# Kernel tuning notes

Hardware: AMD Instinct MI355X
Metric: run time of the kernel (lower is better)

## Reference

```python
import jax, jax.numpy as jnp
import numpy as np

EMBED_DIM = 128
B, N = 8, 2048


def entmax15(z):
    """Exact 1.5-entmax along the last axis (Peters & Martins 2019, sort-based)."""
    z = z / 2.0
    z = z - jnp.max(z, axis=-1, keepdims=True)  # shift-invariance -> numerical stability
    zs = -jnp.sort(-z, axis=-1)                 # descending sort
    n = z.shape[-1]
    k = jnp.arange(1, n + 1, dtype=z.dtype)
    mean = jnp.cumsum(zs, axis=-1) / k
    meansq = jnp.cumsum(zs * zs, axis=-1) / k
    ss = k * (meansq - mean * mean)
    delta = (1.0 - ss) / k
    delta_safe = jnp.where(delta > 0, delta, 1.0)
    tau = mean - jnp.where(delta > 0, jnp.sqrt(delta_safe), 0.0)
    support = jnp.sum((tau <= zs).astype(jnp.int32), axis=-1, keepdims=True)
    tau_star = jnp.take_along_axis(tau, support - 1, axis=-1)
    return jnp.square(jnp.maximum(z - tau_star, 0.0))


def setup_inputs() -> dict:
    key = jax.random.key(0)
    ks = jax.random.split(key, 6)
    s = 1.0 / np.sqrt(EMBED_DIM)  # torch nn.Linear default init range
    return {
        "x_c": jax.random.normal(ks[0], (B, N, EMBED_DIM), jnp.float32),
        "x_n": jax.random.normal(ks[1], (B, N, EMBED_DIM), jnp.float32),
        "Wq": jax.random.uniform(ks[2], (EMBED_DIM, EMBED_DIM), jnp.float32, -s, s),
        "bq": jax.random.uniform(ks[3], (EMBED_DIM,), jnp.float32, -s, s),
        "Wk": jax.random.uniform(ks[4], (EMBED_DIM, EMBED_DIM), jnp.float32, -s, s),
        "bk": jax.random.uniform(ks[5], (EMBED_DIM,), jnp.float32, -s, s),
    }


def reference(x_c, x_n, Wq, bq, Wk, bk):
    Q = x_c @ Wq.T + bq                      # [B,N,D]
    K = x_n @ Wk.T + bk                      # [B,N,D]
    A = jnp.einsum("bnd,bmd->bnm", Q, K) / jnp.sqrt(jnp.float32(EMBED_DIM))
    # entmax15 sparse normalization over keys; dropout is identity in eval mode
    return entmax15(A)
```

## Files before the change

### kernel.cpp

```cpp
#include <hip/hip_runtime.h>
#include <hip/hip_bf16.h>

#define BATCH 8
#define SEQ   2048
#define DIM   128
#define NROWS 16384
#define THETA_SPAN 22.62741699796952f

typedef __bf16    bf16x8   __attribute__((ext_vector_type(8)));
typedef float     floatx16 __attribute__((ext_vector_type(16)));

static __device__ __forceinline__ unsigned short f2bf(float v) {
    union { __hip_bfloat16 h; unsigned short u; } c;
    c.h = __float2bfloat16(v);
    return c.u;
}
static __device__ __forceinline__ float bf2f(unsigned short u) {
    union { unsigned int i; float f; } c;
    c.i = (unsigned int)u << 16;
    return c.f;
}
static __device__ __forceinline__ unsigned short f2h(float v) {
    union { _Float16 h; unsigned short u; } c;
    c.h = (_Float16)v;
    return c.u;
}
static __device__ __forceinline__ float h2f(unsigned short u) {
    union { _Float16 h; unsigned short u; } c;
    c.u = u;
    return (float)c.h;
}

__global__ void __launch_bounds__(256)
proj_qk(const float* __restrict__ xq, const float* __restrict__ xn,
        const float* __restrict__ Wq, const float* __restrict__ bq,
        const float* __restrict__ Wk, const float* __restrict__ bk,
        unsigned short* __restrict__ Qhi, unsigned short* __restrict__ Qlo,
        unsigned short* __restrict__ Kb) {
    const int isK = blockIdx.y;
    const float* __restrict__ X    = isK ? xn : xq;
    const float* __restrict__ W    = isK ? Wk : Wq;
    const float* __restrict__ bias = isK ? bk : bq;

    __shared__ float wt[64][133];
    __shared__ float xs[64][68];
    const int tid  = threadIdx.x;
    const int l    = tid & 15;
    const int kthi = tid >> 4;
    const int row0 = blockIdx.x * 64;

    float s[4][8];
#pragma unroll
    for (int rr = 0; rr < 4; ++rr)
#pragma unroll
        for (int j = 0; j < 8; ++j) s[rr][j] = 0.0f;

    for (int ph = 0; ph < 2; ++ph) {
        const int e0 = ph * 64;
#pragma unroll
        for (int i = 0; i < 8; ++i) {
            const int g  = tid + 256 * i;
            const int d  = g >> 4;
            const int c4 = g & 15;
            float4 wv = *reinterpret_cast<const float4*>(
                W + (size_t)d * DIM + e0 + 4 * c4);
            wt[4*c4+0][d] = wv.x;  wt[4*c4+1][d] = wv.y;
            wt[4*c4+2][d] = wv.z;  wt[4*c4+3][d] = wv.w;
        }
#pragma unroll
        for (int i = 0; i < 4; ++i) {
            const int g  = tid + 256 * i;
            const int r  = g >> 4;
            const int c4 = g & 15;
            float4 xv = *reinterpret_cast<const float4*>(
                X + (size_t)(row0 + r) * DIM + e0 + 4 * c4);
            *reinterpret_cast<float4*>(&xs[r][4 * c4]) = xv;
        }
        __syncthreads();
#pragma unroll 8
        for (int e = 0; e < 64; ++e) {
            float w8[8];
            *reinterpret_cast<float4*>(w8)     =
                *reinterpret_cast<const float4*>(&wt[e][kthi * 8]);
            *reinterpret_cast<float4*>(w8 + 4) =
                *reinterpret_cast<const float4*>(&wt[e][kthi * 8 + 4]);
#pragma unroll
            for (int rr = 0; rr < 4; ++rr) {
                const float xv = xs[l + 16 * rr][e];
#pragma unroll
                for (int j = 0; j < 8; ++j) s[rr][j] = fmaf(xv, w8[j], s[rr][j]);
            }
        }
        __syncthreads();
    }

    float b8[8];
    *reinterpret_cast<float4*>(b8)     = *reinterpret_cast<const float4*>(bias + kthi * 8);
    *reinterpret_cast<float4*>(b8 + 4) = *reinterpret_cast<const float4*>(bias + kthi * 8 + 4);

    if (!isK) {
#pragma unroll
        for (int rr = 0; rr < 4; ++rr) {
            const int row = row0 + l + 16 * rr;
            union { uint4 v; unsigned short u[8]; } ph_, pl_;
#pragma unroll
            for (int j = 0; j < 8; ++j) {
                const float v = s[rr][j] + b8[j];
                const unsigned short h = f2bf(v);
                ph_.u[j] = h;
                pl_.u[j] = f2bf(v - bf2f(h));
            }
            const size_t base = ((size_t)kthi * NROWS + row) * 8;
            *reinterpret_cast<uint4*>(Qhi + base) = ph_.v;
            *reinterpret_cast<uint4*>(Qlo + base) = pl_.v;
        }
    } else {
#pragma unroll
        for (int rr = 0; rr < 4; ++rr) {
            const int row = row0 + l + 16 * rr;
            const int b   = row >> 11;
            const int key = row & (SEQ - 1);
            union { uint4 v; unsigned short u[8]; } pk;
#pragma unroll
            for (int j = 0; j < 8; ++j) pk.u[j] = f2bf(s[rr][j] + b8[j]);
            const size_t base = (((size_t)(b * 16) + kthi) * SEQ + key) * 8;
            *reinterpret_cast<uint4*>(Kb + base) = pk.v;
        }
    }
}

__global__ void __launch_bounds__(256, 3)
score_gemm(const __bf16* __restrict__ Qhi, const __bf16* __restrict__ Qlo,
           const __bf16* __restrict__ Kb, uint2* __restrict__ S4) {
    const int tid  = threadIdx.x;
    const int wv   = tid >> 6;
    const int lane = tid & 63;
    const int l5   = lane & 31;
    const int hi5  = lane >> 5;
    const int row0 = blockIdx.x * 32;
    const int b    = row0 >> 11;
    const int key0 = blockIdx.y * 512 + wv * 128;

    floatx16 acc[4];
    const floatx16 zerov = {};
#pragma unroll
    for (int t = 0; t < 4; ++t) acc[t] = zerov;

    const __bf16* qh = Qhi + ((size_t)hi5 * NROWS + row0 + l5) * 8;
    const __bf16* ql = Qlo + ((size_t)hi5 * NROWS + row0 + l5) * 8;
    const __bf16* kp = Kb + (((size_t)(b * 16) + hi5) * SEQ + key0 + l5) * 8;
    const size_t qstep = (size_t)2 * NROWS * 8;
    const size_t kstep = (size_t)2 * SEQ * 8;

#pragma unroll
    for (int kt = 0; kt < 8; ++kt) {
        const bf16x8 ah = *reinterpret_cast<const bf16x8*>(qh + kt * qstep);
        const bf16x8 al = *reinterpret_cast<const bf16x8*>(ql + kt * qstep);
        const __bf16* kc = kp + kt * kstep;
#pragma unroll
        for (int t = 0; t < 4; ++t) {
            const bf16x8 bkv = *reinterpret_cast<const bf16x8*>(kc + (size_t)t * 256);
            acc[t] = __builtin_amdgcn_mfma_f32_32x32x16_bf16(ah, bkv, acc[t], 0, 0, 0);
            acc[t] = __builtin_amdgcn_mfma_f32_32x32x16_bf16(al, bkv, acc[t], 0, 0, 0);
        }
    }

#pragma unroll
    for (int t = 0; t < 4; ++t) {
#pragma unroll
        for (int a = 0; a < 4; ++a) {
            const int rowgroup = (row0 >> 2) + 2 * a + hi5;
            union { uint2 v; unsigned short u[4]; } pk;
#pragma unroll
            for (int bb = 0; bb < 4; ++bb) pk.u[bb] = f2h(acc[t][4 * a + bb]);
            S4[(size_t)rowgroup * SEQ + key0 + t * 32 + l5] = pk.v;
        }
    }
}

__global__ void __launch_bounds__(256, 4)
entmax_rows(const uint2* __restrict__ S4, float* __restrict__ out) {
    const int lane = threadIdx.x & 63;
    const int w    = threadIdx.x >> 6;
    const int row  = blockIdx.x * 4 + w;
    const int sub  = row & 3;

    const uint2* sp = S4 + (size_t)(row >> 2) * SEQ;
    float z[32];
#pragma unroll
    for (int c = 0; c < 32; ++c) {
        const uint2 v = sp[c * 64 + lane];
        const unsigned int word = (sub & 2) ? v.y : v.x;
        const unsigned short h  = (sub & 1) ? (unsigned short)(word >> 16)
                                            : (unsigned short)(word & 0xffffu);
        z[c] = h2f(h);
    }

    float m = z[0];
#pragma unroll
    for (int i = 1; i < 32; ++i) m = fmaxf(m, z[i]);
#pragma unroll
    for (int off = 32; off >= 1; off >>= 1) m = fmaxf(m, __shfl_xor(m, off, 64));

    float lo = m - THETA_SPAN, hi = m;
    for (int it = 0; it < 12; ++it) {
        const float th = 0.5f * (lo + hi);
        float f0 = 0.0f, f1 = 0.0f, f2 = 0.0f, f3 = 0.0f;
#pragma unroll
        for (int i = 0; i < 8; ++i) {
            const float a0 = fmaxf(z[4 * i + 0] - th, 0.0f);
            const float a1 = fmaxf(z[4 * i + 1] - th, 0.0f);
            const float a2 = fmaxf(z[4 * i + 2] - th, 0.0f);
            const float a3 = fmaxf(z[4 * i + 3] - th, 0.0f);
            f0 = fmaf(a0, a0, f0); f1 = fmaf(a1, a1, f1);
            f2 = fmaf(a2, a2, f2); f3 = fmaf(a3, a3, f3);
        }
        float fs = (f0 + f1) + (f2 + f3);
#pragma unroll
        for (int off = 32; off >= 1; off >>= 1) fs += __shfl_xor(fs, off, 64);
        if (fs >= 512.0f) lo = th; else hi = th;
    }
    const float th = 0.5f * (lo + hi);

    float* orow = out + (size_t)row * SEQ;
#pragma unroll
    for (int c = 0; c < 32; ++c) {
        const float d = fmaxf(z[c] - th, 0.0f);
        orow[c * 64 + lane] = d * d * (1.0f / 512.0f);
    }
}

extern "C" void kernel_launch(void* const* d_in, const int* in_sizes, int n_in,
                              void* d_out, int out_size, void* d_ws, size_t ws_size,
                              hipStream_t stream) {
    const float* x_c = (const float*)d_in[0];
    const float* x_n = (const float*)d_in[1];
    const float* Wq  = (const float*)d_in[2];
    const float* bq  = (const float*)d_in[3];
    const float* Wk  = (const float*)d_in[4];
    const float* bk  = (const float*)d_in[5];
    float* out = (float*)d_out;

    char* ws = (char*)d_ws;
    unsigned short* Qhi = (unsigned short*)ws;
    unsigned short* Qlo = (unsigned short*)(ws + ((size_t)4 << 20));
    unsigned short* Kbl = (unsigned short*)(ws + ((size_t)8 << 20));
    uint2*          S4  = (uint2*)(ws + ((size_t)12 << 20));

    proj_qk<<<dim3(NROWS / 64, 2), 256, 0, stream>>>(
        x_c, x_n, Wq, bq, Wk, bk, Qhi, Qlo, Kbl);
    score_gemm<<<dim3(NROWS / 32, 4), 256, 0, stream>>>(
        (const __bf16*)Qhi, (const __bf16*)Qlo, (const __bf16*)Kbl, S4);
    entmax_rows<<<NROWS / 4, 256, 0, stream>>>(S4, out);
}
```

Before: 209.3 us.

## Fuse score GEMM and entmax into one kernel with LDS-resident fp16 scores

Merges the score GEMM and the entmax row kernel into one 1024-thread block that computes a 32x2048 score tile, keeps it as packed fp16 in shared memory, and runs the bisection directly from LDS. This removes the global round-trip of the fp16 score matrix and one kernel launch. The bisection inner loop now uses packed half2 arithmetic with a dot2 accumulate and one fewer iteration, each wave handling two rows. This trades threshold precision for throughput, and the 128KB LDS per block limits occupancy.

```diff
diff --git a/kernel.cpp b/kernel.cpp
--- a/kernel.cpp
+++ b/kernel.cpp
@@ -9,6 +9,7 @@
 
 typedef __bf16    bf16x8   __attribute__((ext_vector_type(8)));
 typedef float     floatx16 __attribute__((ext_vector_type(16)));
+typedef _Float16  half2v   __attribute__((ext_vector_type(2)));
 
 static __device__ __forceinline__ unsigned short f2bf(float v) {
     union { __hip_bfloat16 h; unsigned short u; } c;
@@ -25,11 +26,16 @@
     c.h = (_Float16)v;
     return c.u;
 }
-static __device__ __forceinline__ float h2f(unsigned short u) {
-    union { _Float16 h; unsigned short u; } c;
-    c.u = u;
-    return (float)c.h;
-}
+
+#if __has_builtin(__builtin_amdgcn_fdot2)
+static __device__ __forceinline__ float fdot2acc(half2v a, half2v b, float c) {
+    return __builtin_amdgcn_fdot2(a, b, c, false);
+}
+#else
+static __device__ __forceinline__ float fdot2acc(half2v a, half2v b, float c) {
+    return fmaf((float)a.y, (float)b.y, fmaf((float)a.x, (float)b.x, c));
+}
+#endif
 
 __global__ void __launch_bounds__(256)
 proj_qk(const float* __restrict__ xq, const float* __restrict__ xn,
@@ -129,9 +135,10 @@
     }
 }
 
-__global__ void __launch_bounds__(256, 3)
-score_gemm(const __bf16* __restrict__ Qhi, const __bf16* __restrict__ Qlo,
-           const __bf16* __restrict__ Kb, uint2* __restrict__ S4) {
+__global__ void __launch_bounds__(1024, 4)
+attn_fused(const __bf16* __restrict__ Qhi, const __bf16* __restrict__ Qlo,
+           const __bf16* __restrict__ Kb, float* __restrict__ out) {
+    __shared__ uint2 S4[8][SEQ];
     const int tid  = threadIdx.x;
     const int wv   = tid >> 6;
     const int lane = tid & 63;
@@ -139,94 +146,105 @@
     const int hi5  = lane >> 5;
     const int row0 = blockIdx.x * 32;
     const int b    = row0 >> 11;
-    const int key0 = blockIdx.y * 512 + wv * 128;
-
-    floatx16 acc[4];
-    const floatx16 zerov = {};
-#pragma unroll
-    for (int t = 0; t < 4; ++t) acc[t] = zerov;
-
-    const __bf16* qh = Qhi + ((size_t)hi5 * NROWS + row0 + l5) * 8;
-    const __bf16* ql = Qlo + ((size_t)hi5 * NROWS + row0 + l5) * 8;
-    const __bf16* kp = Kb + (((size_t)(b * 16) + hi5) * SEQ + key0 + l5) * 8;
-    const size_t qstep = (size_t)2 * NROWS * 8;
-    const size_t kstep = (size_t)2 * SEQ * 8;
-
-#pragma unroll
-    for (int kt = 0; kt < 8; ++kt) {
-        const bf16x8 ah = *reinterpret_cast<const bf16x8*>(qh + kt * qstep);
-        const bf16x8 al = *reinterpret_cast<const bf16x8*>(ql + kt * qstep);
-        const __bf16* kc = kp + kt * kstep;
+    const int key0 = wv * 128;
+
+    {
+        floatx16 acc[4];
+        const floatx16 zerov = {};
+#pragma unroll
+        for (int t = 0; t < 4; ++t) acc[t] = zerov;
+
+        const __bf16* qh = Qhi + ((size_t)hi5 * NROWS + row0 + l5) * 8;
+        const __bf16* ql = Qlo + ((size_t)hi5 * NROWS + row0 + l5) * 8;
+        const __bf16* kp = Kb + (((size_t)(b * 16) + hi5) * SEQ + key0 + l5) * 8;
+        const size_t qstep = (size_t)2 * NROWS * 8;
+        const size_t kstep = (size_t)2 * SEQ * 8;
+
+#pragma unroll
+        for (int kt = 0; kt < 8; ++kt) {
+            const bf16x8 ah = *reinterpret_cast<const bf16x8*>(qh + kt * qstep);
+            const bf16x8 al = *reinterpret_cast<const bf16x8*>(ql + kt * qstep);
+            const __bf16* kc = kp + kt * kstep;
+#pragma unroll
+            for (int t = 0; t < 4; ++t) {
+                const bf16x8 bkv = *reinterpret_cast<const bf16x8*>(kc + (size_t)t * 256);
+                acc[t] = __builtin_amdgcn_mfma_f32_32x32x16_bf16(ah, bkv, acc[t], 0, 0, 0);
+                acc[t] = __builtin_amdgcn_mfma_f32_32x32x16_bf16(al, bkv, acc[t], 0, 0, 0);
+            }
+        }
 #pragma unroll
         for (int t = 0; t < 4; ++t) {
-            const bf16x8 bkv = *reinterpret_cast<const bf16x8*>(kc + (size_t)t * 256);
-            acc[t] = __builtin_amdgcn_mfma_f32_32x32x16_bf16(ah, bkv, acc[t], 0, 0, 0);
-            acc[t] = __builtin_amdgcn_mfma_f32_32x32x16_bf16(al, bkv, acc[t], 0, 0, 0);
-        }
-    }
-
-#pragma unroll
-    for (int t = 0; t < 4; ++t) {
-#pragma unroll
-        for (int a = 0; a < 4; ++a) {
-            const int rowgroup = (row0 >> 2) + 2 * a + hi5;
-            union { uint2 v; unsigned short u[4]; } pk;
-#pragma unroll
-            for (int bb = 0; bb < 4; ++bb) pk.u[bb] = f2h(acc[t][4 * a + bb]);
-            S4[(size_t)rowgroup * SEQ + key0 + t * 32 + l5] = pk.v;
-        }
-    }
-}
-
-__global__ void __launch_bounds__(256, 4)
-entmax_rows(const uint2* __restrict__ S4, float* __restrict__ out) {
-    const int lane = threadIdx.x & 63;
-    const int w    = threadIdx.x >> 6;
-    const int row  = blockIdx.x * 4 + w;
-    const int sub  = row & 3;
-
-    const uint2* sp = S4 + (size_t)(row >> 2) * SEQ;
-    float z[32];
-#pragma unroll
-    for (int c = 0; c < 32; ++c) {
-        const uint2 v = sp[c * 64 + lane];
-        const unsigned int word = (sub & 2) ? v.y : v.x;
-        const unsigned short h  = (sub & 1) ? (unsigned short)(word >> 16)
-                                            : (unsigned short)(word & 0xffffu);
-        z[c] = h2f(h);
-    }
-
-    float m = z[0];
-#pragma unroll
-    for (int i = 1; i < 32; ++i) m = fmaxf(m, z[i]);
-#pragma unroll
-    for (int off = 32; off >= 1; off >>= 1) m = fmaxf(m, __shfl_xor(m, off, 64));
-
-    float lo = m - THETA_SPAN, hi = m;
-    for (int it = 0; it < 12; ++it) {
-        const float th = 0.5f * (lo + hi);
-        float f0 = 0.0f, f1 = 0.0f, f2 = 0.0f, f3 = 0.0f;
-#pragma unroll
-        for (int i = 0; i < 8; ++i) {
-            const float a0 = fmaxf(z[4 * i + 0] - th, 0.0f);
-            const float a1 = fmaxf(z[4 * i + 1] - th, 0.0f);
-            const float a2 = fmaxf(z[4 * i + 2] - th, 0.0f);
-            const float a3 = fmaxf(z[4 * i + 3] - th, 0.0f);
-            f0 = fmaf(a0, a0, f0); f1 = fmaf(a1, a1, f1);
-            f2 = fmaf(a2, a2, f2); f3 = fmaf(a3, a3, f3);
-        }
-        float fs = (f0 + f1) + (f2 + f3);
-#pragma unroll
-        for (int off = 32; off >= 1; off >>= 1) fs += __shfl_xor(fs, off, 64);
-        if (fs >= 512.0f) lo = th; else hi = th;
-    }
-    const float th = 0.5f * (lo + hi);
-
-    float* orow = out + (size_t)row * SEQ;
-#pragma unroll
-    for (int c = 0; c < 32; ++c) {
-        const float d = fmaxf(z[c] - th, 0.0f);
-        orow[c * 64 + lane] = d * d * (1.0f / 512.0f);
+#pragma unroll
+            for (int a = 0; a < 4; ++a) {
+                union { uint2 v; unsigned short u[4]; } pk;
+#pragma unroll
+                for (int bb = 0; bb < 4; ++bb) pk.u[bb] = f2h(acc[t][4 * a + bb]);
+                S4[2 * a + hi5][key0 + t * 32 + l5] = pk.v;
+            }
+        }
+    }
+    __syncthreads();
+
+    const int g  = wv >> 1;
+    const int sp = wv & 1;
+
+    const unsigned int* Sw = reinterpret_cast<const unsigned int*>(&S4[g][0]);
+    unsigned int raw[32];
+#pragma unroll
+    for (int c = 0; c < 32; ++c) raw[c] = Sw[2 * (c * 64 + lane) + sp];
+
+    const half2v hzero = {(_Float16)0.0f, (_Float16)0.0f};
+
+#pragma unroll
+    for (int s = 0; s < 2; ++s) {
+        half2v z[16];
+#pragma unroll
+        for (int i = 0; i < 16; ++i) {
+            const unsigned int merged = __builtin_amdgcn_perm(
+                raw[2 * i + 1], raw[2 * i],
+                s ? 0x07060302u : 0x05040100u);
+            union { unsigned int u; half2v h; } cv;
+            cv.u = merged;
+            z[i] = cv.h;
+        }
+
+        float m = -1e30f;
+#pragma unroll
+        for (int i = 0; i < 16; ++i)
+            m = fmaxf(m, fmaxf((float)z[i].x, (float)z[i].y));
+#pragma unroll
+        for (int off = 32; off >= 1; off >>= 1)
+            m = fmaxf(m, __shfl_xor(m, off, 64));
+
+        float lo = m - THETA_SPAN, hi = m;
+        float th = 0.0f;
+        for (int it = 0; it < 11; ++it) {
+            th = 0.5f * (lo + hi);
+            const _Float16 thh = (_Float16)th;
+            const half2v nth2 = {(_Float16)-thh, (_Float16)-thh};
+            float f = 0.0f;
+#pragma unroll
+            for (int i = 0; i < 16; ++i) {
+                half2v d = z[i] + nth2;
+                d = __builtin_elementwise_max(d, hzero);
+                f = fdot2acc(d, d, f);
+            }
+#pragma unroll
+            for (int off = 32; off >= 1; off >>= 1)
+                f += __shfl_xor(f, off, 64);
+            if (f >= 512.0f) lo = th; else hi = th;
+        }
+        th = 0.5f * (lo + hi);
+        th = (float)((_Float16)th);
+
+        float* orow = out + (size_t)(row0 + 4 * g + 2 * sp + s) * SEQ + lane;
+#pragma unroll
+        for (int i = 0; i < 16; ++i) {
+            const float d0 = fmaxf((float)z[i].x - th, 0.0f);
+            const float d1 = fmaxf((float)z[i].y - th, 0.0f);
+            orow[(size_t)(2 * i) * 64]     = d0 * d0 * (1.0f / 512.0f);
+            orow[(size_t)(2 * i + 1) * 64] = d1 * d1 * (1.0f / 512.0f);
+        }
     }
 }
 
@@ -245,11 +263,9 @@
     unsigned short* Qhi = (unsigned short*)ws;
     unsigned short* Qlo = (unsigned short*)(ws + ((size_t)4 << 20));
     unsigned short* Kbl = (unsigned short*)(ws + ((size_t)8 << 20));
-    uint2*          S4  = (uint2*)(ws + ((size_t)12 << 20));
 
     proj_qk<<<dim3(NROWS / 64, 2), 256, 0, stream>>>(
         x_c, x_n, Wq, bq, Wk, bk, Qhi, Qlo, Kbl);
-    score_gemm<<<dim3(NROWS / 32, 4), 256, 0, stream>>>(
-        (const __bf16*)Qhi, (const __bf16*)Qlo, (const __bf16*)Kbl, S4);
-    entmax_rows<<<NROWS / 4, 256, 0, stream>>>(S4, out);
-}
+    attn_fused<<<NROWS / 32, 1024, 0, stream>>>(
+        (const __bf16*)Qhi, (const __bf16*)Qlo, (const __bf16*)Kbl, out);
+}
```

After: 200.7 us. 1.04x faster.
